# Kernel optimization log

Measured on AMD Instinct MI355X. Metric: run time of the kernel, lower is better.

## Reference

```python
import jax, jax.numpy as jnp
import numpy as np

B = 16384
H = 1024

def setup_inputs() -> dict:
    key = jax.random.key(0)
    k1, k2, k3, k4, k5 = jax.random.split(key, 5)
    inp = jax.random.normal(k1, (B, 3 * H), dtype=jnp.float32)
    previous_state = jax.random.normal(k2, (B, H), dtype=jnp.float32)
    mask = jax.random.uniform(k3, (B,), dtype=jnp.float32)
    # params: th_normal scale 0.08
    Wur = 0.08 * jax.random.normal(k4, (H, 2 * H), dtype=jnp.float32)
    U = 0.08 * jax.random.normal(k5, (H, H), dtype=jnp.float32)
    return {"inp": inp, "previous_state": previous_state, "mask": mask, "Wur": Wur, "U": U}

def reference(inp, previous_state, mask, Wur, U):
    h = U.shape[0]
    state_inp = inp[:, :h]            # [B, H]
    gate_inp = inp[:, h:]             # [B, 2H]
    gates = jax.nn.sigmoid(previous_state @ Wur + gate_inp)  # [B, 2H]
    update = gates[:, :h]
    reset = gates[:, h:]
    p = (state_inp * reset) @ U       # [B, H]
    next_state = jnp.tanh(p + state_inp)
    # NOTE: faithful to source (additive combine, not convex blend)
    next_state_f = next_state + update + (previous_state + (1.0 - update))
    m = mask[:, None]
    return m * next_state_f + (1.0 - m) * previous_state
```

## Files before the change

kernel.cpp:

```cpp
#include <hip/hip_runtime.h>
#include <cstdint>
#include <cstddef>

#define DI __device__ __forceinline__

typedef __attribute__((ext_vector_type(8))) short short8;
typedef __attribute__((ext_vector_type(4))) float floatx4;

static constexpr int BATCH = 16384;
static constexpr int H = 1024;

DI unsigned short f32_to_bf16_bits(float x) {
  union { float f; unsigned int u; } c; c.f = x;
  unsigned int r = c.u + 0x7fffu + ((c.u >> 16) & 1u);
  return (unsigned short)(r >> 16);
}

__global__ __launch_bounds__(256) void cast_bf16_kernel(const float* __restrict__ in,
                                                        unsigned short* __restrict__ out) {
  const int i = (blockIdx.x * 256 + threadIdx.x) * 4;
  const float4 v = *reinterpret_cast<const float4*>(in + i);
  ushort4 o;
  o.x = f32_to_bf16_bits(v.x);
  o.y = f32_to_bf16_bits(v.y);
  o.z = f32_to_bf16_bits(v.z);
  o.w = f32_to_bf16_bits(v.w);
  *reinterpret_cast<ushort4*>(out + i) = o;
}

__global__ __launch_bounds__(256) void transpose_cast_kernel(const float* __restrict__ in,
                                                             unsigned short* __restrict__ out,
                                                             int src_stride, int src_col0) {
  __shared__ float tile[32][33];
  const int bx = blockIdx.x * 32;
  const int by = blockIdx.y * 32;
  const int tx = threadIdx.x;
  const int ty = threadIdx.y;
#pragma unroll
  for (int i = 0; i < 32; i += 8)
    tile[ty + i][tx] = in[(size_t)(bx + ty + i) * src_stride + src_col0 + by + tx];
  __syncthreads();
#pragma unroll
  for (int i = 0; i < 32; i += 8)
    out[(size_t)(by + ty + i) * H + bx + tx] = f32_to_bf16_bits(tile[tx][ty + i]);
}

template <int EPI>
__global__ __launch_bounds__(256, 2) void gemm_fused(const unsigned short* __restrict__ A,
                                                     const unsigned short* __restrict__ Bt,
                                                     const float* __restrict__ inp,
                                                     const float* __restrict__ prev,
                                                     const float* __restrict__ mask,
                                                     unsigned short* __restrict__ Xout,
                                                     float* __restrict__ Out) {
  __shared__ __align__(16) unsigned short ldsA[128 * 64];
  __shared__ __align__(16) unsigned short ldsB[128 * 64];

  const int tid = threadIdx.x;
  const int lane = tid & 63;
  const int wave = tid >> 6;
  const int wm = wave >> 1;
  const int wn = wave & 1;
  const int q = lane >> 4;
  const int l16 = lane & 15;
  const int blockM = blockIdx.y * 128;
  const int blockN = blockIdx.x * 128;

  floatx4 acc[4][4] = {};

  for (int kt = 0; kt < H; kt += 64) {
#pragma unroll
    for (int j = 0; j < 4; ++j) {
      const int c = j * 256 + tid;
      const int r = c >> 3;
      const int gc = (c & 7) ^ (r & 7);
      const int cb = j * 256 + (wave << 6);
      const unsigned short* srcA = A + (size_t)(blockM + r) * H + kt + gc * 8;
      const unsigned short* srcB = Bt + (size_t)(blockN + r) * H + kt + gc * 8;
#if __has_builtin(__builtin_amdgcn_global_load_lds)
      __builtin_amdgcn_global_load_lds(
          (const __attribute__((address_space(1))) unsigned int*)srcA,
          (__attribute__((address_space(3))) unsigned int*)(&ldsA[cb * 8]), 16, 0, 0);
      __builtin_amdgcn_global_load_lds(
          (const __attribute__((address_space(1))) unsigned int*)srcB,
          (__attribute__((address_space(3))) unsigned int*)(&ldsB[cb * 8]), 16, 0, 0);
#else
      *(short8*)&ldsA[c * 8] = *(const short8*)srcA;
      *(short8*)&ldsB[c * 8] = *(const short8*)srcB;
#endif
    }
#if __has_builtin(__builtin_amdgcn_global_load_lds)
    asm volatile("s_waitcnt vmcnt(0)" ::: "memory");
#endif
    __syncthreads();

#pragma unroll
    for (int ks = 0; ks < 2; ++ks) {
      short8 af[4], bfr[4];
#pragma unroll
      for (int i = 0; i < 4; ++i) {
        const int r = wm * 64 + i * 16 + l16;
        const int ch = ks * 4 + q;
        af[i] = *(const short8*)&ldsA[(r * 8 + (ch ^ (r & 7))) * 8];
      }
#pragma unroll
      for (int j = 0; j < 4; ++j) {
        const int r = wn * 64 + j * 16 + l16;
        const int ch = ks * 4 + q;
        bfr[j] = *(const short8*)&ldsB[(r * 8 + (ch ^ (r & 7))) * 8];
      }
#pragma unroll
      for (int i = 0; i < 4; ++i)
#pragma unroll
        for (int j = 0; j < 4; ++j)
          acc[i][j] = __builtin_amdgcn_mfma_f32_16x16x32_bf16(af[i], bfr[j], acc[i][j], 0, 0, 0);
    }
    __syncthreads();
  }

#pragma unroll
  for (int i = 0; i < 4; ++i) {
    const int gr0 = blockM + wm * 64 + i * 16 + q * 4;
#pragma unroll
    for (int j = 0; j < 4; ++j) {
      const int gcol = blockN + wn * 64 + j * 16 + l16;
#pragma unroll
      for (int rg = 0; rg < 4; ++rg) {
        const int gr = gr0 + rg;
        const float v = acc[i][j][rg];
        if (EPI == 0) {
          const float z = v + inp[(size_t)gr * (3 * H) + 2 * H + gcol];
          const float rst = 1.0f / (1.0f + __expf(-z));
          const float x = inp[(size_t)gr * (3 * H) + gcol] * rst;
          Xout[(size_t)gr * H + gcol] = f32_to_bf16_bits(x);
        } else {
          const float s = inp[(size_t)gr * (3 * H) + gcol];
          const float a = v + s;
          const float ns = 1.0f - 2.0f / (__expf(2.0f * a) + 1.0f);
          const float m = mask[gr];
          Out[(size_t)gr * H + gcol] = m * (ns + 1.0f) + prev[(size_t)gr * H + gcol];
        }
      }
    }
  }
}

extern "C" void kernel_launch(void* const* d_in, const int* in_sizes, int n_in,
                              void* d_out, int out_size, void* d_ws, size_t ws_size,
                              hipStream_t stream) {
  const float* inp = (const float*)d_in[0];
  const float* prev = (const float*)d_in[1];
  const float* mask = (const float*)d_in[2];
  const float* Wur = (const float*)d_in[3];
  const float* U = (const float*)d_in[4];
  float* out = (float*)d_out;

  char* ws = (char*)d_ws;
  unsigned short* prevb = (unsigned short*)ws;
  unsigned short* Xb = (unsigned short*)(ws + (size_t)BATCH * H * 2);
  unsigned short* WrT = (unsigned short*)(ws + (size_t)BATCH * H * 4);
  unsigned short* UT = WrT + (size_t)H * H;

  cast_bf16_kernel<<<(BATCH * H) / (256 * 4), 256, 0, stream>>>(prev, prevb);
  transpose_cast_kernel<<<dim3(H / 32, H / 32), dim3(32, 8), 0, stream>>>(Wur, WrT, 2 * H, H);
  transpose_cast_kernel<<<dim3(H / 32, H / 32), dim3(32, 8), 0, stream>>>(U, UT, H, 0);

  gemm_fused<0><<<dim3(H / 128, BATCH / 128), 256, 0, stream>>>(prevb, WrT, inp, nullptr,
                                                                nullptr, Xb, nullptr);
  gemm_fused<1><<<dim3(H / 128, BATCH / 128), 256, 0, stream>>>(Xb, UT, inp, prev, mask,
                                                                nullptr, out);
}
```

Before: 443.7 us.

## Remap GEMM workgroups per XCD, raise occupancy, fuse transpose launches

```diff
diff --git a/kernel.cpp b/kernel.cpp
--- a/kernel.cpp
+++ b/kernel.cpp
@@ -18,20 +18,34 @@
 
 __global__ __launch_bounds__(256) void cast_bf16_kernel(const float* __restrict__ in,
                                                         unsigned short* __restrict__ out) {
-  const int i = (blockIdx.x * 256 + threadIdx.x) * 4;
-  const float4 v = *reinterpret_cast<const float4*>(in + i);
-  ushort4 o;
-  o.x = f32_to_bf16_bits(v.x);
-  o.y = f32_to_bf16_bits(v.y);
-  o.z = f32_to_bf16_bits(v.z);
-  o.w = f32_to_bf16_bits(v.w);
-  *reinterpret_cast<ushort4*>(out + i) = o;
+  const int i = (blockIdx.x * 256 + threadIdx.x) * 8;
+  const float4 v0 = *reinterpret_cast<const float4*>(in + i);
+  const float4 v1 = *reinterpret_cast<const float4*>(in + i + 4);
+  short8 o;
+  o[0] = (short)f32_to_bf16_bits(v0.x);
+  o[1] = (short)f32_to_bf16_bits(v0.y);
+  o[2] = (short)f32_to_bf16_bits(v0.z);
+  o[3] = (short)f32_to_bf16_bits(v0.w);
+  o[4] = (short)f32_to_bf16_bits(v1.x);
+  o[5] = (short)f32_to_bf16_bits(v1.y);
+  o[6] = (short)f32_to_bf16_bits(v1.z);
+  o[7] = (short)f32_to_bf16_bits(v1.w);
+  *reinterpret_cast<short8*>(out + i) = o;
 }
 
-__global__ __launch_bounds__(256) void transpose_cast_kernel(const float* __restrict__ in,
-                                                             unsigned short* __restrict__ out,
-                                                             int src_stride, int src_col0) {
+__global__ __launch_bounds__(256) void transpose_cast2_kernel(const float* __restrict__ Wur,
+                                                              const float* __restrict__ U,
+                                                              unsigned short* __restrict__ WrT,
+                                                              unsigned short* __restrict__ UT) {
   __shared__ float tile[32][33];
+  const float* in;
+  unsigned short* out;
+  int src_stride, src_col0;
+  if (blockIdx.z == 0) {
+    in = Wur; out = WrT; src_stride = 2 * H; src_col0 = H;
+  } else {
+    in = U; out = UT; src_stride = H; src_col0 = 0;
+  }
   const int bx = blockIdx.x * 32;
   const int by = blockIdx.y * 32;
   const int tx = threadIdx.x;
@@ -46,7 +60,7 @@
 }
 
 template <int EPI>
-__global__ __launch_bounds__(256, 2) void gemm_fused(const unsigned short* __restrict__ A,
+__global__ __launch_bounds__(256, 3) void gemm_fused(const unsigned short* __restrict__ A,
                                                      const unsigned short* __restrict__ Bt,
                                                      const float* __restrict__ inp,
                                                      const float* __restrict__ prev,
@@ -63,8 +77,14 @@
   const int wn = wave & 1;
   const int q = lane >> 4;
   const int l16 = lane & 15;
-  const int blockM = blockIdx.y * 128;
-  const int blockN = blockIdx.x * 128;
+
+  const int sid = blockIdx.y * gridDim.x + blockIdx.x;
+  const int nwg = gridDim.x * gridDim.y;
+  const int lid = (sid & 7) * (nwg >> 3) + (sid >> 3);
+  const int bx = lid & 7;
+  const int by = lid >> 3;
+  const int blockM = by * 128;
+  const int blockN = bx * 128;
 
   floatx4 acc[4][4] = {};
 
@@ -161,9 +181,8 @@
   unsigned short* WrT = (unsigned short*)(ws + (size_t)BATCH * H * 4);
   unsigned short* UT = WrT + (size_t)H * H;
 
-  cast_bf16_kernel<<<(BATCH * H) / (256 * 4), 256, 0, stream>>>(prev, prevb);
-  transpose_cast_kernel<<<dim3(H / 32, H / 32), dim3(32, 8), 0, stream>>>(Wur, WrT, 2 * H, H);
-  transpose_cast_kernel<<<dim3(H / 32, H / 32), dim3(32, 8), 0, stream>>>(U, UT, H, 0);
+  cast_bf16_kernel<<<(BATCH * H) / (256 * 8), 256, 0, stream>>>(prev, prevb);
+  transpose_cast2_kernel<<<dim3(H / 32, H / 32, 2), dim3(32, 8), 0, stream>>>(Wur, U, WrT, UT);
 
   gemm_fused<0><<<dim3(H / 128, BATCH / 128), 256, 0, stream>>>(prevb, WrT, inp, nullptr,
                                                                 nullptr, Xb, nullptr);
```

Result: faster. 427.2 us (-3.7%).
